# Kernel tuning notes

Hardware: AMD Instinct MI355X
Metric: run time of the kernel (lower is better)

## Reference

```python
import jax, jax.numpy as jnp
from jax import lax
import numpy as np

NUM_HEADS = 8
KW = 3  # window kernel size

def _avgpool3(x):
    # x: [B,C,H,W]; AvgPool2d(3,1,1) with count_include_pad=True -> sum/9
    s = lax.reduce_window(x, 0.0, lax.add, (1, 1, KW, KW), (1, 1, 1, 1),
                          ((0, 0), (0, 0), (1, 1), (1, 1)))
    return s / (KW * KW)

def _unfold3(y):
    # y: [B,h,w,C] -> [B,h,w,9,C]; patch index ordered row-major (kh,kw)
    B, h, w, C = y.shape
    yp = jnp.pad(y, ((0, 0), (1, 1), (1, 1), (0, 0)))
    return jnp.stack([yp[:, i:i + h, j:j + w, :]
                      for i in range(KW) for j in range(KW)], axis=3)

def setup_inputs():
    key = jax.random.key(0)
    ks = jax.random.split(key, 9)
    B, C, H, W = 8, 256, 64, 64
    sd = 0.02
    return {
        "x": jax.random.normal(ks[0], (B, C, H, W), jnp.float32),
        "W_qkv": jax.random.normal(ks[1], (4 * C, C), jnp.float32) * sd,
        "b_qkv": jnp.zeros((4 * C,), jnp.float32),
        "W1": jax.random.normal(ks[2], (C // 2, C), jnp.float32) * sd,
        "b1": jnp.zeros((C // 2,), jnp.float32),
        "W2": jax.random.normal(ks[3], (C, C // 2), jnp.float32) * sd,
        "b2": jnp.zeros((C,), jnp.float32),
        "Wp": jax.random.normal(ks[4], (C, C), jnp.float32) * sd,
        "bp": jnp.zeros((C,), jnp.float32),
    }

def reference(x, W_qkv, b_qkv, W1, b1, W2, b2, Wp, bp):
    B, C, H, W = x.shape
    nH = NUM_HEADS
    hd = C // nH
    scale = hd ** -0.5
    # avg pool (stride 1 keeps spatial dims), to channels-last
    y = _avgpool3(x).transpose(0, 2, 3, 1)                 # [B,h,w,C]
    qkv = y @ W_qkv.T + b_qkv                              # [B,h,w,4C]
    qkv = qkv.reshape(B, H, W, C, 4)
    q, k, v, chans = qkv[..., 0], qkv[..., 1], qkv[..., 2], qkv[..., 3]
    # channel gate
    g = jax.nn.sigmoid(jax.nn.relu(chans @ W1.T + b1) @ W2.T + b2)  # [B,h,w,C]
    # local window attention: each query attends to its 3x3 neighborhood
    qh = q.reshape(B, H, W, nH, hd)                        # [B,h,w,n,d]
    kp = _unfold3(k).reshape(B, H, W, KW * KW, nH, hd)     # [B,h,w,9,n,d]
    vp = _unfold3(v).reshape(B, H, W, KW * KW, nH, hd)
    attn = jnp.einsum('bhwnd,bhwknd->bhwnk', qh, kp) * scale
    attn = jax.nn.softmax(attn, axis=-1)
    out = jnp.einsum('bhwnk,bhwknd->bhwnd', attn, vp).reshape(B, H, W, C)
    out = out * g + out
    out = out @ Wp.T + bp
    return out.transpose(0, 3, 1, 2)                       # [B,C,H,W]
```

## Files before the change

kernel.cpp:

```cpp
#include <hip/hip_runtime.h>
#include <stdint.h>

typedef __bf16    bf16x8 __attribute__((ext_vector_type(8)));
typedef float     f32x4  __attribute__((ext_vector_type(4)));
typedef uint32_t  u32x4  __attribute__((ext_vector_type(4)));

#define MFMA(a,b,c) __builtin_amdgcn_mfma_f32_16x16x32_bf16((a),(b),(c),0,0,0)

__device__ __align__(16) uint16_t g_y [8*64*64*256];
__device__ __align__(16) uint16_t g_wpk[393216];

#define WQF 0
#define WKF 65536
#define WVF 131072
#define WCF 196608
#define W1F 262144
#define W2F 294912
#define WPF 327680

static __device__ __forceinline__ float b2f(uint32_t u){ return __builtin_bit_cast(float, u<<16); }
static __device__ __forceinline__ uint32_t f2b(float f){
  uint32_t x = __builtin_bit_cast(uint32_t, f);
  return (x + 0x7fffu + ((x>>16)&1u)) >> 16;
}
static __device__ __forceinline__ uint16_t f2bn(float f){
  return __builtin_bit_cast(uint16_t, (__bf16)f);
}
static __device__ __forceinline__ uint32_t pk2(float x, float y){
  return (uint32_t)f2bn(x) | ((uint32_t)f2bn(y) << 16);
}

__global__ __launch_bounds__(512) void kprep(const float* __restrict__ x,
    const float* __restrict__ Wqkv, const float* __restrict__ W1,
    const float* __restrict__ W2, const float* __restrict__ Wp){
  int t = threadIdx.x;
  int bid = blockIdx.x;
  if (bid < 512){
    __shared__ __align__(16) uint16_t sm[6*64*82];
    uint32_t* smw = (uint32_t*)sm;
    int b = bid >> 6, rem = bid & 63;
    int hg = rem >> 2, cg = rem & 3;
    int h0 = hg*4, ch = cg*64;
    for (int i=t; i<384; i+=512){
      int base = i*41;
      smw[base+3]  = 0;
      smw[base+36] = 0;
    }
    if (hg==0){
      for (int i=t; i<2624; i+=512) smw[i] = 0;
    }
    if (hg==15){
      for (int i=t; i<2624; i+=512) smw[5*2624 + i] = 0;
    }
    #pragma unroll
    for (int i=0;i<12;i++){
      int id = t + 512*i;
      int w4 = id&15, c = (id>>4)&63, hh = id>>10;
      int gy = h0 - 1 + hh;
      if ((unsigned)gy < 64u){
        f32x4 ld = *(const f32x4*)&x[(((b*256+ch+c)*64+gy)*64) + w4*4];
        int wb = (((hh*64+c)*82 + 8 + w4*4) >> 1);
        smw[wb+0] = pk2(ld[0], ld[1]);
        smw[wb+1] = pk2(ld[2], ld[3]);
      }
    }
    __syncthreads();
    int c = t & 63, wsel = (t >> 6) & 1, py = t >> 7;
    int r0 = ((py+0)*64+c)*82, r1 = ((py+1)*64+c)*82, r2 = ((py+2)*64+c)*82;
    int w0 = wsel*32;
    float csp = b2f(sm[r0+w0+7]) + b2f(sm[r1+w0+7]) + b2f(sm[r2+w0+7]);
    float csc = b2f(sm[r0+w0+8]) + b2f(sm[r1+w0+8]) + b2f(sm[r2+w0+8]);
    uint16_t* dst = g_y + ((b*64 + h0 + py)*64)*256 + ch + c;
    for (int j2=0;j2<32;j2++){
      int w = w0 + j2;
      float csn = b2f(sm[r0+w+9]) + b2f(sm[r1+w+9]) + b2f(sm[r2+w+9]);
      float yv = (csp + csc + csn) * (1.0f/9.0f);
      dst[w*256] = f2bn(yv);
      csp = csc; csc = csn;
    }
  } else {
    int idx = (bid - 512)*512 + t;
    int j = idx & 7, lane = (idx>>3)&63;
    int n16 = lane & 15, q4 = lane>>4;
    float v;
    if (idx < 262144){
      int tt = idx >> 16, l = idx & 65535;
      int s = (l>>9)&7, nt = l>>12;
      v = Wqkv[(4*(nt*16+n16) + tt)*256 + s*32 + q4*8 + j];
    } else if (idx < 294912){
      int l = idx - 262144;
      int s = (l>>9)&7, nt = l>>12;
      v = W1[(nt*16+n16)*256 + s*32 + q4*8 + j];
    } else if (idx < 327680){
      int l = idx - 294912;
      int s = (l>>9)&3, nt = l>>11;
      v = W2[(nt*16+n16)*128 + s*32 + q4*8 + j];
    } else {
      int l = idx - 327680;
      int s = (l>>9)&7, nt = l>>12;
      v = Wp[(nt*16+n16)*256 + s*32 + q4*8 + j];
    }
    g_wpk[idx] = f2bn(v);
  }
}

#define YSTR  264
#define HSTR  136
#define K2_QS 15840
#define K2_KS 20192
#define K2_VS 28352
#define MCH   0
#define MHS   8448
#define MAO   15840
#define MAOSTR 266
__global__ __launch_bounds__(512,4) void kattn(const float* __restrict__ bqkv,
    const float* __restrict__ b1, const float* __restrict__ b2v,
    const float* __restrict__ bp, float* __restrict__ out){
  __shared__ __align__(16) uint16_t sm[36512];
  int t = threadIdx.x;
  int lane = t & 63, wave = t >> 6;
  int n16 = lane & 15, quad = lane >> 4;
  int bid = blockIdx.x;
  int bb = bid >> 7, ty = (bid >> 3) & 15, tx = bid & 7;

  uint32_t opk[2][8];
  uint32_t chp[16];

  #pragma unroll
  for (int i=0;i<4;i++){
    int id = t + 512*i;
    if (id < 1920){
      int hp = id >> 5, c8 = id & 31;
      int py = hp/10, px = hp - py*10;
      int gy = ty*4 + py - 1, gx = tx*8 + px - 1;
      u32x4 ld = {0,0,0,0};
      if ((unsigned)gy<64u && (unsigned)gx<64u)
        ld = *(const u32x4*)&g_y[((bb*64+gy)*64+gx)*256 + c8*8];
      *(u32x4*)&sm[hp*YSTR + c8*8] = ld;
    }
  }
  __syncthreads();

  #pragma unroll
  for (int hf=0; hf<2; hf++){
    {
      int ntg = hf*8 + wave;
      bf16x8 Bq[8];
      #pragma unroll
      for (int s=0;s<8;s++) Bq[s] = *(const bf16x8*)&g_wpk[WQF + ((ntg*8+s)*64+lane)*8];
      float bq = bqkv[4*(ntg*16+n16) + 0];
      int colB = wave*16;
      #pragma unroll
      for (int mt=0; mt<2; mt++){
        f32x4 a = {0.f,0.f,0.f,0.f};
        int m = mt*16 + n16;
        int hrow = 10*(m>>3) + (m&7) + 11;
        #pragma unroll
        for (int s=0;s<8;s++){
          bf16x8 A = *(const bf16x8*)&sm[hrow*YSTR + s*32 + quad*8];
          a = MFMA(A, Bq[s], a);
        }
        #pragma unroll
        for (int r=0;r<4;r++){
          int row = mt*16 + quad*4 + r;
          sm[K2_QS + row*HSTR + colB + n16] = (uint16_t)f2b(a[r] + bq);
        }
      }
    }
    {
      int ntg = hf*8 + wave;
      bf16x8 Bk[8], Bv[8];
      #pragma unroll
      for (int s=0;s<8;s++){
        Bk[s] = *(const bf16x8*)&g_wpk[WKF + ((ntg*8+s)*64+lane)*8];
        Bv[s] = *(const bf16x8*)&g_wpk[WVF + ((ntg*8+s)*64+lane)*8];
      }
      float bk = bqkv[4*(ntg*16+n16) + 1];
      float bv = bqkv[4*(ntg*16+n16) + 2];
      int colB = wave*16;
      #pragma unroll
      for (int mt=0; mt<4; mt++){
        f32x4 ak = {0.f,0.f,0.f,0.f}, av = {0.f,0.f,0.f,0.f};
        int m = mt*16 + n16;
        int mr = (m < 60) ? m : 59;
        #pragma unroll
        for (int s=0;s<8;s++){
          bf16x8 A = *(const bf16x8*)&sm[mr*YSTR + s*32 + quad*8];
          ak = MFMA(A, Bk[s], ak);
          av = MFMA(A, Bv[s], av);
        }
        #pragma unroll
        for (int r=0;r<4;r++){
          int row = mt*16 + quad*4 + r;
          if (row < 60){
            int py = row/10, px = row - py*10;
            int gy = ty*4 + py - 1, gx = tx*8 + px - 1;
            bool ok = ((unsigned)gy<64u) && ((unsigned)gx<64u);
            float vk = ok ? ak[r] + bk : 0.f;
            float vv = ok ? av[r] + bv : 0.f;
            sm[K2_KS + row*HSTR + colB + n16] = (uint16_t)f2b(vk);
            sm[K2_VS + row*HSTR + colB + n16] = (uint16_t)f2b(vv);
          }
        }
      }
    }
    __syncthreads();
    if (wave < 4){
      int p = lane & 31, half = lane >> 5;
      int cb = wave*32 + half*16;
      const uint16_t* qp = &sm[K2_QS + p*HSTR + cb];
      u32x4 qa = *(const u32x4*)qp;
      u32x4 qb = *(const u32x4*)(qp+8);
      float qv[16];
      #pragma unroll
      for (int i=0;i<4;i++){
        qv[2*i]    = b2f(qa[i]&0xffffu); qv[2*i+1]   = b2f(qa[i]>>16);
        qv[8+2*i]  = b2f(qb[i]&0xffffu); qv[8+2*i+1] = b2f(qb[i]>>16);
      }
      int hb = 10*(p>>3) + (p&7) + 11;
      const int off[9] = {-11,-10,-9,-1,0,1,9,10,11};
      float sc[9];
      #pragma unroll
      for (int nb=0;nb<9;nb++){
        const uint16_t* kp = &sm[K2_KS + (hb+off[nb])*HSTR + cb];
        u32x4 ka = *(const u32x4*)kp;
        u32x4 kb = *(const u32x4*)(kp+8);
        float s = 0.f;
        #pragma unroll
        for (int i=0;i<4;i++){
          s += qv[2*i]*b2f(ka[i]&0xffffu)   + qv[2*i+1]*b2f(ka[i]>>16);
          s += qv[8+2*i]*b2f(kb[i]&0xffffu) + qv[8+2*i+1]*b2f(kb[i]>>16);
        }
        s += __shfl_xor(s, 32);
        sc[nb] = s * 0.17677669529663687f;
      }
      float mx = sc[0];
      #pragma unroll
      for (int nb=1;nb<9;nb++) mx = fmaxf(mx, sc[nb]);
      float l = 0.f;
      #pragma unroll
      for (int nb=0;nb<9;nb++){ sc[nb] = __expf(sc[nb]-mx); l += sc[nb]; }
      float inv = 1.f / l;
      float o[16];
      #pragma unroll
      for (int i=0;i<16;i++) o[i]=0.f;
      #pragma unroll
      for (int nb=0;nb<9;nb++){
        float wgt = sc[nb]*inv;
        const uint16_t* vp = &sm[K2_VS + (hb+off[nb])*HSTR + cb];
        u32x4 va = *(const u32x4*)vp;
        u32x4 vb = *(const u32x4*)(vp+8);
        #pragma unroll
        for (int i=0;i<4;i++){
          o[2*i]    += wgt*b2f(va[i]&0xffffu); o[2*i+1]   += wgt*b2f(va[i]>>16);
          o[8+2*i]  += wgt*b2f(vb[i]&0xffffu); o[8+2*i+1] += wgt*b2f(vb[i]>>16);
        }
      }
      #pragma unroll
      for (int i=0;i<8;i++) opk[hf][i] = f2b(o[2*i]) | (f2b(o[2*i+1])<<16);
    } else if (hf == 0){
      #pragma unroll
      for (int jj=0;jj<4;jj++){
        int ntg = (wave-4)*4 + jj;
        bf16x8 Bc[8];
        #pragma unroll
        for (int s=0;s<8;s++) Bc[s] = *(const bf16x8*)&g_wpk[WCF + ((ntg*8+s)*64+lane)*8];
        float bc = bqkv[4*(ntg*16+n16) + 3];
        #pragma unroll
        for (int mt=0; mt<2; mt++){
          f32x4 a = {0.f,0.f,0.f,0.f};
          int m = mt*16 + n16;
          int hrow = 10*(m>>3) + (m&7) + 11;
          #pragma unroll
          for (int s=0;s<8;s++){
            bf16x8 A = *(const bf16x8*)&sm[hrow*YSTR + s*32 + quad*8];
            a = MFMA(A, Bc[s], a);
          }
          chp[(jj*2+mt)*2+0] = f2b(a[0]+bc) | (f2b(a[1]+bc)<<16);
          chp[(jj*2+mt)*2+1] = f2b(a[2]+bc) | (f2b(a[3]+bc)<<16);
        }
      }
    } else {
      #pragma unroll
      for (int jj=0;jj<4;jj++){
        int ntg = (wave-4)*4 + jj;
        int col = ntg*16 + n16;
        #pragma unroll
        for (int mt=0;mt<2;mt++){
          #pragma unroll
          for (int r2=0;r2<2;r2++){
            uint32_t v = chp[(jj*2+mt)*2+r2];
            int row = mt*16 + quad*4 + r2*2;
            sm[MCH + row*264 + col]     = (uint16_t)(v & 0xffffu);
            sm[MCH + (row+1)*264 + col] = (uint16_t)(v >> 16);
          }
        }
      }
    }
    __syncthreads();
  }
  if (wave < 4){
    int p = lane & 31, half = lane >> 5;
    int cb = wave*32 + half*16;
    #pragma unroll
    for (int hf=0;hf<2;hf++)
      #pragma unroll
      for (int i=0;i<8;i++)
        *(uint32_t*)&sm[MAO + p*MAOSTR + hf*128 + cb + 2*i] = opk[hf][i];
  }
  {
    int ntg = wave;
    bf16x8 Bf[8];
    #pragma unroll
    for (int s=0;s<8;s++) Bf[s] = *(const bf16x8*)&g_wpk[W1F + ((ntg*8+s)*64+lane)*8];
    float bs = b1[ntg*16+n16];
    int colB = wave*16;
    #pragma unroll
    for (int mt=0;mt<2;mt++){
      f32x4 a = {0.f,0.f,0.f,0.f};
      #pragma unroll
      for (int s=0;s<8;s++){
        bf16x8 A = *(const bf16x8*)&sm[MCH + (mt*16+n16)*264 + s*32 + quad*8];
        a = MFMA(A, Bf[s], a);
      }
      #pragma unroll
      for (int r=0;r<4;r++){
        int row = mt*16 + quad*4 + r;
        sm[MHS + row*HSTR + colB + n16] = (uint16_t)f2b(fmaxf(a[r]+bs, 0.f));
      }
    }
  }
  __syncthreads();
  #pragma unroll
  for (int jj=0;jj<2;jj++){
    int ntg = wave*2 + jj;
    bf16x8 Bf[4];
    #pragma unroll
    for (int s=0;s<4;s++) Bf[s] = *(const bf16x8*)&g_wpk[W2F + ((ntg*4+s)*64+lane)*8];
    float bs = b2v[ntg*16+n16];
    int colB = ntg*16;
    #pragma unroll
    for (int mt=0;mt<2;mt++){
      f32x4 a = {0.f,0.f,0.f,0.f};
      #pragma unroll
      for (int s=0;s<4;s++){
        bf16x8 A = *(const bf16x8*)&sm[MHS + (mt*16+n16)*HSTR + s*32 + quad*8];
        a = MFMA(A, Bf[s], a);
      }
      #pragma unroll
      for (int r=0;r<4;r++){
        int row = mt*16 + quad*4 + r;
        float gg = 1.f/(1.f+__expf(-(a[r] + bs)));
        float ao = b2f((uint32_t)sm[MAO + row*MAOSTR + colB + n16]);
        sm[MCH + row*264 + colB + n16] = (uint16_t)f2b(ao*(1.f+gg));
      }
    }
  }
  __syncthreads();
  #pragma unroll
  for (int jj=0;jj<2;jj++){
    int ntg = wave*2 + jj;
    bf16x8 Bf[8];
    #pragma unroll
    for (int s=0;s<8;s++) Bf[s] = *(const bf16x8*)&g_wpk[WPF + ((ntg*8+s)*64+lane)*8];
    float bs = bp[ntg*16+n16];
    int colB = ntg*16;
    #pragma unroll
    for (int mt=0;mt<2;mt++){
      f32x4 a = {0.f,0.f,0.f,0.f};
      #pragma unroll
      for (int s=0;s<8;s++){
        bf16x8 A = *(const bf16x8*)&sm[MCH + (mt*16+n16)*264 + s*32 + quad*8];
        a = MFMA(A, Bf[s], a);
      }
      #pragma unroll
      for (int r=0;r<4;r++){
        int row = mt*16 + quad*4 + r;
        sm[MAO + row*MAOSTR + colB + n16] = (uint16_t)f2b(a[r]+bs);
      }
    }
  }
  __syncthreads();
  #pragma unroll
  for (int i=0;i<4;i++){
    int idx = t + 512*i;
    int ix4 = idx&1, iy = (idx>>1)&3, c = idx>>3;
    f32x4 stv;
    #pragma unroll
    for (int j=0;j<4;j++){
      int p = iy*8 + ix4*4 + j;
      stv[j] = b2f((uint32_t)sm[MAO + p*MAOSTR + c]);
    }
    *(f32x4*)&out[(((bb*256+c)*64) + ty*4+iy)*64 + tx*8 + ix4*4] = stv;
  }
}

extern "C" void kernel_launch(void* const* d_in, const int* in_sizes, int n_in,
                              void* d_out, int out_size, void* d_ws, size_t ws_size,
                              hipStream_t stream){
  (void)in_sizes; (void)n_in; (void)d_ws; (void)ws_size; (void)out_size;
  const float* x    = (const float*)d_in[0];
  const float* Wqkv = (const float*)d_in[1];
  const float* bqkv = (const float*)d_in[2];
  const float* W1   = (const float*)d_in[3];
  const float* b1   = (const float*)d_in[4];
  const float* W2   = (const float*)d_in[5];
  const float* b2   = (const float*)d_in[6];
  const float* Wp   = (const float*)d_in[7];
  const float* bp   = (const float*)d_in[8];
  kprep<<<dim3(1280), dim3(512), 0, stream>>>(x, Wqkv, W1, W2, Wp);
  kattn<<<dim3(1024), dim3(512), 0, stream>>>(bqkv, b1, b2, bp, (float*)d_out);
}
```

Baseline: 176.3 us.

## Use hardware bf16 conversion, transpose output staging, and interleave MFMA chains

Swaps the software round-to-nearest bf16 conversion for native __bf16 casts and unpacks high halves with a mask instead of a shift. Restructures the channel-gate, W2 and projection GEMMs so two N-tiles and both M-tiles accumulate together, which shares A and B fragment loads and gives the MFMA pipe independent chains. The final projection result is stored transposed (channel-major) in LDS so the output store reads packed 8-byte values instead of four scalar LDS reads. These target ALU overhead and LDS traffic, in exchange for more live accumulator registers.

```diff
diff --git a/kernel.cpp b/kernel.cpp
--- a/kernel.cpp
+++ b/kernel.cpp
@@ -4,6 +4,7 @@
 typedef __bf16    bf16x8 __attribute__((ext_vector_type(8)));
 typedef float     f32x4  __attribute__((ext_vector_type(4)));
 typedef uint32_t  u32x4  __attribute__((ext_vector_type(4)));
+typedef uint32_t  u32x2  __attribute__((ext_vector_type(2)));
 
 #define MFMA(a,b,c) __builtin_amdgcn_mfma_f32_16x16x32_bf16((a),(b),(c),0,0,0)
 
@@ -19,10 +20,8 @@
 #define WPF 327680
 
 static __device__ __forceinline__ float b2f(uint32_t u){ return __builtin_bit_cast(float, u<<16); }
-static __device__ __forceinline__ uint32_t f2b(float f){
-  uint32_t x = __builtin_bit_cast(uint32_t, f);
-  return (x + 0x7fffu + ((x>>16)&1u)) >> 16;
-}
+static __device__ __forceinline__ float blo(uint32_t u){ return __builtin_bit_cast(float, u<<16); }
+static __device__ __forceinline__ float bhi(uint32_t u){ return __builtin_bit_cast(float, u & 0xffff0000u); }
 static __device__ __forceinline__ uint16_t f2bn(float f){
   return __builtin_bit_cast(uint16_t, (__bf16)f);
 }
@@ -113,6 +112,8 @@
 #define MHS   8448
 #define MAO   15840
 #define MAOSTR 266
+#define MAOT  15840
+#define MTSTR 36
 __global__ __launch_bounds__(512,4) void kattn(const float* __restrict__ bqkv,
     const float* __restrict__ b1, const float* __restrict__ b2v,
     const float* __restrict__ bp, float* __restrict__ out){
@@ -125,6 +126,9 @@
 
   uint32_t opk[2][8];
   uint32_t chp[16];
+
+  int hrow0 = 10*(n16>>3) + (n16&7) + 11;
+  int hrow1 = hrow0 + 20;
 
   #pragma unroll
   for (int i=0;i<4;i++){
@@ -153,8 +157,7 @@
       #pragma unroll
       for (int mt=0; mt<2; mt++){
         f32x4 a = {0.f,0.f,0.f,0.f};
-        int m = mt*16 + n16;
-        int hrow = 10*(m>>3) + (m&7) + 11;
+        int hrow = mt ? hrow1 : hrow0;
         #pragma unroll
         for (int s=0;s<8;s++){
           bf16x8 A = *(const bf16x8*)&sm[hrow*YSTR + s*32 + quad*8];
@@ -163,7 +166,7 @@
         #pragma unroll
         for (int r=0;r<4;r++){
           int row = mt*16 + quad*4 + r;
-          sm[K2_QS + row*HSTR + colB + n16] = (uint16_t)f2b(a[r] + bq);
+          sm[K2_QS + row*HSTR + colB + n16] = f2bn(a[r] + bq);
         }
       }
     }
@@ -196,10 +199,8 @@
             int py = row/10, px = row - py*10;
             int gy = ty*4 + py - 1, gx = tx*8 + px - 1;
             bool ok = ((unsigned)gy<64u) && ((unsigned)gx<64u);
-            float vk = ok ? ak[r] + bk : 0.f;
-            float vv = ok ? av[r] + bv : 0.f;
-            sm[K2_KS + row*HSTR + colB + n16] = (uint16_t)f2b(vk);
-            sm[K2_VS + row*HSTR + colB + n16] = (uint16_t)f2b(vv);
+            sm[K2_KS + row*HSTR + colB + n16] = ok ? f2bn(ak[r] + bk) : (uint16_t)0;
+            sm[K2_VS + row*HSTR + colB + n16] = ok ? f2bn(av[r] + bv) : (uint16_t)0;
           }
         }
       }
@@ -214,8 +215,8 @@
       float qv[16];
       #pragma unroll
       for (int i=0;i<4;i++){
-        qv[2*i]    = b2f(qa[i]&0xffffu); qv[2*i+1]   = b2f(qa[i]>>16);
-        qv[8+2*i]  = b2f(qb[i]&0xffffu); qv[8+2*i+1] = b2f(qb[i]>>16);
+        qv[2*i]    = blo(qa[i]); qv[2*i+1]   = bhi(qa[i]);
+        qv[8+2*i]  = blo(qb[i]); qv[8+2*i+1] = bhi(qb[i]);
       }
       int hb = 10*(p>>3) + (p&7) + 11;
       const int off[9] = {-11,-10,-9,-1,0,1,9,10,11};
@@ -228,8 +229,8 @@
         float s = 0.f;
         #pragma unroll
         for (int i=0;i<4;i++){
-          s += qv[2*i]*b2f(ka[i]&0xffffu)   + qv[2*i+1]*b2f(ka[i]>>16);
-          s += qv[8+2*i]*b2f(kb[i]&0xffffu) + qv[8+2*i+1]*b2f(kb[i]>>16);
+          s += qv[2*i]*blo(ka[i])   + qv[2*i+1]*bhi(ka[i]);
+          s += qv[8+2*i]*blo(kb[i]) + qv[8+2*i+1]*bhi(kb[i]);
         }
         s += __shfl_xor(s, 32);
         sc[nb] = s * 0.17677669529663687f;
@@ -252,32 +253,39 @@
         u32x4 vb = *(const u32x4*)(vp+8);
         #pragma unroll
         for (int i=0;i<4;i++){
-          o[2*i]    += wgt*b2f(va[i]&0xffffu); o[2*i+1]   += wgt*b2f(va[i]>>16);
-          o[8+2*i]  += wgt*b2f(vb[i]&0xffffu); o[8+2*i+1] += wgt*b2f(vb[i]>>16);
-        }
-      }
-      #pragma unroll
-      for (int i=0;i<8;i++) opk[hf][i] = f2b(o[2*i]) | (f2b(o[2*i+1])<<16);
+          o[2*i]    += wgt*blo(va[i]); o[2*i+1]   += wgt*bhi(va[i]);
+          o[8+2*i]  += wgt*blo(vb[i]); o[8+2*i+1] += wgt*bhi(vb[i]);
+        }
+      }
+      #pragma unroll
+      for (int i=0;i<8;i++) opk[hf][i] = pk2(o[2*i], o[2*i+1]);
     } else if (hf == 0){
+      f32x4 cc[4][2];
+      #pragma unroll
+      for (int jj=0;jj<4;jj++){
+        cc[jj][0] = f32x4{0.f,0.f,0.f,0.f};
+        cc[jj][1] = f32x4{0.f,0.f,0.f,0.f};
+      }
+      #pragma unroll
+      for (int s=0;s<8;s++){
+        bf16x8 A0 = *(const bf16x8*)&sm[hrow0*YSTR + s*32 + quad*8];
+        bf16x8 A1 = *(const bf16x8*)&sm[hrow1*YSTR + s*32 + quad*8];
+        #pragma unroll
+        for (int jj=0;jj<4;jj++){
+          int ntg = (wave-4)*4 + jj;
+          bf16x8 Bc = *(const bf16x8*)&g_wpk[WCF + ((ntg*8+s)*64+lane)*8];
+          cc[jj][0] = MFMA(A0, Bc, cc[jj][0]);
+          cc[jj][1] = MFMA(A1, Bc, cc[jj][1]);
+        }
+      }
       #pragma unroll
       for (int jj=0;jj<4;jj++){
         int ntg = (wave-4)*4 + jj;
-        bf16x8 Bc[8];
-        #pragma unroll
-        for (int s=0;s<8;s++) Bc[s] = *(const bf16x8*)&g_wpk[WCF + ((ntg*8+s)*64+lane)*8];
         float bc = bqkv[4*(ntg*16+n16) + 3];
         #pragma unroll
-        for (int mt=0; mt<2; mt++){
-          f32x4 a = {0.f,0.f,0.f,0.f};
-          int m = mt*16 + n16;
-          int hrow = 10*(m>>3) + (m&7) + 11;
-          #pragma unroll
-          for (int s=0;s<8;s++){
-            bf16x8 A = *(const bf16x8*)&sm[hrow*YSTR + s*32 + quad*8];
-            a = MFMA(A, Bc[s], a);
-          }
-          chp[(jj*2+mt)*2+0] = f2b(a[0]+bc) | (f2b(a[1]+bc)<<16);
-          chp[(jj*2+mt)*2+1] = f2b(a[2]+bc) | (f2b(a[3]+bc)<<16);
+        for (int mt=0;mt<2;mt++){
+          chp[(jj*2+mt)*2+0] = pk2(cc[jj][mt][0]+bc, cc[jj][mt][1]+bc);
+          chp[(jj*2+mt)*2+1] = pk2(cc[jj][mt][2]+bc, cc[jj][mt][3]+bc);
         }
       }
     } else {
@@ -326,57 +334,67 @@
       #pragma unroll
       for (int r=0;r<4;r++){
         int row = mt*16 + quad*4 + r;
-        sm[MHS + row*HSTR + colB + n16] = (uint16_t)f2b(fmaxf(a[r]+bs, 0.f));
+        sm[MHS + row*HSTR + colB + n16] = f2bn(fmaxf(a[r]+bs, 0.f));
       }
     }
   }
   __syncthreads();
-  #pragma unroll
-  for (int jj=0;jj<2;jj++){
-    int ntg = wave*2 + jj;
-    bf16x8 Bf[4];
-    #pragma unroll
-    for (int s=0;s<4;s++) Bf[s] = *(const bf16x8*)&g_wpk[W2F + ((ntg*4+s)*64+lane)*8];
-    float bs = b2v[ntg*16+n16];
-    int colB = ntg*16;
-    #pragma unroll
-    for (int mt=0;mt<2;mt++){
-      f32x4 a = {0.f,0.f,0.f,0.f};
-      #pragma unroll
-      for (int s=0;s<4;s++){
-        bf16x8 A = *(const bf16x8*)&sm[MHS + (mt*16+n16)*HSTR + s*32 + quad*8];
-        a = MFMA(A, Bf[s], a);
-      }
-      #pragma unroll
-      for (int r=0;r<4;r++){
-        int row = mt*16 + quad*4 + r;
-        float gg = 1.f/(1.f+__expf(-(a[r] + bs)));
-        float ao = b2f((uint32_t)sm[MAO + row*MAOSTR + colB + n16]);
-        sm[MCH + row*264 + colB + n16] = (uint16_t)f2b(ao*(1.f+gg));
+  {
+    int nt0 = wave*2, nt1 = nt0+1;
+    f32x4 g00={0.f,0.f,0.f,0.f}, g01={0.f,0.f,0.f,0.f};
+    f32x4 g10={0.f,0.f,0.f,0.f}, g11={0.f,0.f,0.f,0.f};
+    #pragma unroll
+    for (int s=0;s<4;s++){
+      bf16x8 B0 = *(const bf16x8*)&g_wpk[W2F + ((nt0*4+s)*64+lane)*8];
+      bf16x8 B1 = *(const bf16x8*)&g_wpk[W2F + ((nt1*4+s)*64+lane)*8];
+      bf16x8 A0 = *(const bf16x8*)&sm[MHS + n16*HSTR + s*32 + quad*8];
+      bf16x8 A1 = *(const bf16x8*)&sm[MHS + (16+n16)*HSTR + s*32 + quad*8];
+      g00 = MFMA(A0,B0,g00); g01 = MFMA(A1,B0,g01);
+      g10 = MFMA(A0,B1,g10); g11 = MFMA(A1,B1,g11);
+    }
+    float bs0 = b2v[nt0*16+n16], bs1 = b2v[nt1*16+n16];
+    #pragma unroll
+    for (int jj=0;jj<2;jj++){
+      int colB = (wave*2+jj)*16;
+      float bs = jj ? bs1 : bs0;
+      #pragma unroll
+      for (int mt=0;mt<2;mt++){
+        f32x4 a = jj ? (mt ? g11 : g10) : (mt ? g01 : g00);
+        #pragma unroll
+        for (int r=0;r<4;r++){
+          int row = mt*16 + quad*4 + r;
+          float gg = 1.f/(1.f+__expf(-(a[r] + bs)));
+          float ao = b2f((uint32_t)sm[MAO + row*MAOSTR + colB + n16]);
+          sm[MCH + row*264 + colB + n16] = f2bn(ao*(1.f+gg));
+        }
       }
     }
   }
   __syncthreads();
-  #pragma unroll
-  for (int jj=0;jj<2;jj++){
-    int ntg = wave*2 + jj;
-    bf16x8 Bf[8];
-    #pragma unroll
-    for (int s=0;s<8;s++) Bf[s] = *(const bf16x8*)&g_wpk[WPF + ((ntg*8+s)*64+lane)*8];
-    float bs = bp[ntg*16+n16];
-    int colB = ntg*16;
-    #pragma unroll
-    for (int mt=0;mt<2;mt++){
-      f32x4 a = {0.f,0.f,0.f,0.f};
-      #pragma unroll
-      for (int s=0;s<8;s++){
-        bf16x8 A = *(const bf16x8*)&sm[MCH + (mt*16+n16)*264 + s*32 + quad*8];
-        a = MFMA(A, Bf[s], a);
-      }
-      #pragma unroll
-      for (int r=0;r<4;r++){
-        int row = mt*16 + quad*4 + r;
-        sm[MAO + row*MAOSTR + colB + n16] = (uint16_t)f2b(a[r]+bs);
+  {
+    int nt0 = wave*2, nt1 = nt0+1;
+    f32x4 p00={0.f,0.f,0.f,0.f}, p01={0.f,0.f,0.f,0.f};
+    f32x4 p10={0.f,0.f,0.f,0.f}, p11={0.f,0.f,0.f,0.f};
+    #pragma unroll
+    for (int s=0;s<8;s++){
+      bf16x8 B0 = *(const bf16x8*)&g_wpk[WPF + ((nt0*8+s)*64+lane)*8];
+      bf16x8 B1 = *(const bf16x8*)&g_wpk[WPF + ((nt1*8+s)*64+lane)*8];
+      bf16x8 A0 = *(const bf16x8*)&sm[MCH + n16*264 + s*32 + quad*8];
+      bf16x8 A1 = *(const bf16x8*)&sm[MCH + (16+n16)*264 + s*32 + quad*8];
+      p00 = MFMA(A0,B0,p00); p01 = MFMA(A1,B0,p01);
+      p10 = MFMA(A0,B1,p10); p11 = MFMA(A1,B1,p11);
+    }
+    float bs0 = bp[nt0*16+n16], bs1 = bp[nt1*16+n16];
+    #pragma unroll
+    for (int jj=0;jj<2;jj++){
+      int col = (wave*2+jj)*16 + n16;
+      float bs = jj ? bs1 : bs0;
+      #pragma unroll
+      for (int mt=0;mt<2;mt++){
+        f32x4 a = jj ? (mt ? p11 : p10) : (mt ? p01 : p00);
+        u32x2 pk = { pk2(a[0]+bs, a[1]+bs), pk2(a[2]+bs, a[3]+bs) };
+        int row0 = mt*16 + quad*4;
+        *(u32x2*)&sm[MAOT + col*MTSTR + row0] = pk;
       }
     }
   }
@@ -385,12 +403,11 @@
   for (int i=0;i<4;i++){
     int idx = t + 512*i;
     int ix4 = idx&1, iy = (idx>>1)&3, c = idx>>3;
+    int p0 = iy*8 + ix4*4;
+    u32x2 pk = *(const u32x2*)&sm[MAOT + c*MTSTR + p0];
     f32x4 stv;
-    #pragma unroll
-    for (int j=0;j<4;j++){
-      int p = iy*8 + ix4*4 + j;
-      stv[j] = b2f((uint32_t)sm[MAO + p*MAOSTR + c]);
-    }
+    stv[0] = blo(pk[0]); stv[1] = bhi(pk[0]);
+    stv[2] = blo(pk[1]); stv[3] = bhi(pk[1]);
     *(f32x4*)&out[(((bb*256+c)*64) + ty*4+iy)*64 + tx*8 + ix4*4] = stv;
   }
 }
```

Measured after the change: 175.9 us. No clear change (-0.2%).
